# Optimization experiments

Hardware: AMD Instinct MI355X
Metric: run time of the kernel (lower is better)

Reference implementation:

```python
import jax, jax.numpy as jnp
import numpy as np

SINK = 4          # sink_size: tokens never evicted
MAX_CACHE = 8192  # sink_size + window_size
H = 32            # n_heads
HD = 128          # head_dim
D = H * HD        # d_model


def setup_inputs() -> dict:
    key = jax.random.key(0)
    ks = jax.random.split(key, 7)
    x = jax.random.normal(ks[0], (1, 1, D), dtype=jnp.float32)
    cached_k = jax.random.normal(ks[1], (1, H, MAX_CACHE, HD), dtype=jnp.float32)
    cached_v = jax.random.normal(ks[2], (1, H, MAX_CACHE, HD), dtype=jnp.float32)
    scale = 0.02
    Wq = jax.random.normal(ks[3], (D, D), dtype=jnp.float32) * scale
    Wk = jax.random.normal(ks[4], (D, D), dtype=jnp.float32) * scale
    Wv = jax.random.normal(ks[5], (D, D), dtype=jnp.float32) * scale
    Wo = jax.random.normal(ks[6], (D, D), dtype=jnp.float32) * scale
    return {"x": x, "cached_k": cached_k, "cached_v": cached_v,
            "Wq": Wq, "Wk": Wk, "Wv": Wv, "Wo": Wo}


def reference(x, cached_k, cached_v, Wq, Wk, Wv, Wo):
    """One StreamingLLM decode step with a full sink+window KV cache.

    x:        (1, 1, D)   single new token
    cached_k: (1, H, T, HD) with T == MAX_CACHE (cache at capacity)
    Returns (out, new_cached_k, new_cached_v) where out is (1, 1, D) and the
    new caches reflect sink-preserving eviction: [sink | recent[1:] | new].
    """
    B, S, _ = x.shape  # S == 1
    # projections for the new token -> (B, H, S, HD)
    q = (x @ Wq).reshape(B, S, H, HD).transpose(0, 2, 1, 3)
    k_new = (x @ Wk).reshape(B, S, H, HD).transpose(0, 2, 1, 3)
    v_new = (x @ Wv).reshape(B, S, H, HD).transpose(0, 2, 1, 3)

    # attend over past cache + new token (causal: single query sees everything)
    keys = jnp.concatenate([cached_k, k_new], axis=2)   # (B, H, T+1, HD)
    vals = jnp.concatenate([cached_v, v_new], axis=2)
    inv_sqrt_d = np.float32(1.0 / np.sqrt(HD))
    scores = jnp.einsum('bhqd,bhkd->bhqk', q, keys) * inv_sqrt_d
    attn = jax.nn.softmax(scores, axis=-1)
    ctx = jnp.einsum('bhqk,bhkd->bhqd', attn, vals)     # (B, H, 1, HD)
    out = ctx.transpose(0, 2, 1, 3).reshape(B, S, H * HD) @ Wo

    # KVCache.update full-cache branch: keep sink, drop oldest recent, append new
    new_cached_k = jnp.concatenate(
        [cached_k[:, :, :SINK], cached_k[:, :, SINK + 1:], k_new], axis=2)
    new_cached_v = jnp.concatenate(
        [cached_v[:, :, :SINK], cached_v[:, :, SINK + 1:], v_new], axis=2)
    return out, new_cached_k, new_cached_v
```

## Files before the change

kernel.cpp:

```cpp
#include <hip/hip_runtime.h>

#define D     4096
#define NH    32
#define HD    128
#define TT    8192
#define SINKN 4
#define NC    64
#define CS    (TT / NC)
#define ICH   32
#define ICHO  64

__global__ void qkv_partial(const float* __restrict__ x,
                            const float* __restrict__ Wq,
                            const float* __restrict__ Wk,
                            const float* __restrict__ Wv,
                            float* __restrict__ partA) {
    int bid = blockIdx.x;
    int mat = bid / 256;
    int rem = bid % 256;
    int jb  = rem >> 5;
    int ic  = rem & 31;
    const float* Wm = (mat == 0) ? Wq : (mat == 1) ? Wk : Wv;
    int tid = threadIdx.x;
    int j0  = jb * 512 + tid * 4;
    int i0  = ic * 128;
    __shared__ float xs[128];
    xs[tid] = x[i0 + tid];
    __syncthreads();
    float4 acc = {0.f, 0.f, 0.f, 0.f};
    const float* Wp = Wm + (size_t)i0 * D + j0;
    #pragma unroll 8
    for (int i = 0; i < 128; ++i) {
        float4 w = *(const float4*)Wp;
        float xv = xs[i];
        acc.x += xv * w.x; acc.y += xv * w.y;
        acc.z += xv * w.z; acc.w += xv * w.w;
        Wp += D;
    }
    *(float4*)(partA + (size_t)(mat * ICH + ic) * D + j0) = acc;
}

__global__ void attn_chunk(const float* __restrict__ partA,
                           const float* __restrict__ K,
                           const float* __restrict__ V,
                           float* __restrict__ newK,
                           float* __restrict__ newV,
                           float* __restrict__ partB) {
    int bid = blockIdx.x;
    int h = bid / NC;
    int c = bid % NC;
    int t0 = c * CS;
    int tid  = threadIdx.x;
    int wave = tid >> 6;
    int lane = tid & 63;
    int l31  = lane & 31;
    int half = lane >> 5;

    __shared__ float qs[HD];
    __shared__ float sc[CS];
    __shared__ float ml[2];
    __shared__ float ctx8[8][HD];

    {
        int d  = tid & 127;
        int hh = tid >> 7;
        const float* p = partA + (size_t)(hh * 16) * D + (size_t)h * HD + d;
        float s = 0.f;
        #pragma unroll
        for (int ic = 0; ic < 16; ++ic) s += p[(size_t)ic * D];
        ctx8[hh][d] = s;
    }
    __syncthreads();
    if (tid < HD) qs[tid] = ctx8[0][tid] + ctx8[1][tid];
    __syncthreads();

    float4 qv = *(const float4*)(qs + 4 * l31);
    const float scale = 0.08838834764831845f;

    const float* Kh = K    + (size_t)h * TT * HD;
    float*      nKh = newK + (size_t)h * TT * HD;
    for (int kk = 0; kk < 16; ++kk) {
        int r = t0 + kk * 8 + wave * 2 + half;
        float4 kv = *(const float4*)(Kh + (size_t)r * HD + 4 * l31);
        float p = qv.x * kv.x + qv.y * kv.y + qv.z * kv.z + qv.w * kv.w;
        p += __shfl_xor(p, 16, 64);
        p += __shfl_xor(p, 8, 64);
        p += __shfl_xor(p, 4, 64);
        p += __shfl_xor(p, 2, 64);
        p += __shfl_xor(p, 1, 64);
        if (l31 == 0) sc[r - t0] = p * scale;
        if (r != SINKN) {
            int dst = (r < SINKN) ? r : r - 1;
            *(float4*)(nKh + (size_t)dst * HD + 4 * l31) = kv;
        }
    }
    __syncthreads();
    if (wave == 0) {
        float s0 = sc[lane], s1 = sc[lane + 64];
        float m = fmaxf(s0, s1);
        #pragma unroll
        for (int off = 32; off; off >>= 1) m = fmaxf(m, __shfl_xor(m, off, 64));
        float w0 = __expf(s0 - m), w1 = __expf(s1 - m);
        sc[lane] = w0; sc[lane + 64] = w1;
        float l = w0 + w1;
        #pragma unroll
        for (int off = 32; off; off >>= 1) l += __shfl_xor(l, off, 64);
        if (lane == 0) { ml[0] = m; ml[1] = l; }
    }
    __syncthreads();
    const float* Vh = V    + (size_t)h * TT * HD;
    float*      nVh = newV + (size_t)h * TT * HD;
    float a0 = 0.f, a1 = 0.f, a2 = 0.f, a3 = 0.f;
    for (int kk = 0; kk < 16; ++kk) {
        int r = t0 + kk * 8 + wave * 2 + half;
        float4 vv = *(const float4*)(Vh + (size_t)r * HD + 4 * l31);
        float w = sc[r - t0];
        a0 += w * vv.x; a1 += w * vv.y; a2 += w * vv.z; a3 += w * vv.w;
        if (r != SINKN) {
            int dst = (r < SINKN) ? r : r - 1;
            *(float4*)(nVh + (size_t)dst * HD + 4 * l31) = vv;
        }
    }
    int g = wave * 2 + half;
    ctx8[g][4 * l31 + 0] = a0;
    ctx8[g][4 * l31 + 1] = a1;
    ctx8[g][4 * l31 + 2] = a2;
    ctx8[g][4 * l31 + 3] = a3;
    __syncthreads();
    float* pb = partB + ((size_t)h * NC + c) * (HD + 2);
    if (tid < HD) {
        float s = 0.f;
        #pragma unroll
        for (int gg = 0; gg < 8; ++gg) s += ctx8[gg][tid];
        pb[2 + tid] = s;
    }
    if (tid == 0) { pb[0] = ml[0]; pb[1] = ml[1]; }
}

__global__ void attn_combine(const float* __restrict__ partA,
                             const float* __restrict__ partB,
                             float* __restrict__ newK,
                             float* __restrict__ newV,
                             float* __restrict__ ctx) {
    int h = blockIdx.x;
    int tid = threadIdx.x;
    float qd = 0.f, kd = 0.f, vd = 0.f;
    const float* pq = partA + (size_t)h * HD + tid;
    #pragma unroll
    for (int ic = 0; ic < ICH; ++ic) {
        qd += pq[(size_t)ic * D];
        kd += pq[(size_t)(ICH + ic) * D];
        vd += pq[(size_t)(2 * ICH + ic) * D];
    }
    newK[((size_t)h * TT + (TT - 1)) * HD + tid] = kd;
    newV[((size_t)h * TT + (TT - 1)) * HD + tid] = vd;

    __shared__ float red[HD];
    __shared__ float marr[NC], larr[NC], earr[NC];
    red[tid] = qd * kd;
    __syncthreads();
    for (int s = 64; s > 0; s >>= 1) {
        if (tid < s) red[tid] += red[tid + s];
        __syncthreads();
    }
    float s_new = red[0] * 0.08838834764831845f;
    const float* pb = partB + (size_t)h * NC * (HD + 2);
    if (tid < NC) {
        marr[tid] = pb[(size_t)tid * (HD + 2)];
        larr[tid] = pb[(size_t)tid * (HD + 2) + 1];
    }
    __syncthreads();
    float M = s_new;
    for (int c = 0; c < NC; ++c) M = fmaxf(M, marr[c]);
    if (tid < NC) earr[tid] = __expf(marr[tid] - M);
    __syncthreads();
    float wn = __expf(s_new - M);
    float L = wn;
    for (int c = 0; c < NC; ++c) L += larr[c] * earr[c];
    float acc = wn * vd;
    for (int c = 0; c < NC; ++c)
        acc += earr[c] * pb[(size_t)c * (HD + 2) + 2 + tid];
    ctx[h * HD + tid] = acc / L;
}

__global__ void out_partial(const float* __restrict__ ctx,
                            const float* __restrict__ Wo,
                            float* __restrict__ partC) {
    int bid = blockIdx.x;
    int jb = bid >> 6;
    int ic = bid & 63;
    int tid = threadIdx.x;
    int j0 = jb * 512 + tid * 4;
    int i0 = ic * 64;
    __shared__ float xs[64];
    if (tid < 64) xs[tid] = ctx[i0 + tid];
    __syncthreads();
    float4 acc = {0.f, 0.f, 0.f, 0.f};
    const float* Wp = Wo + (size_t)i0 * D + j0;
    #pragma unroll 8
    for (int i = 0; i < 64; ++i) {
        float4 w = *(const float4*)Wp;
        float xv = xs[i];
        acc.x += xv * w.x; acc.y += xv * w.y;
        acc.z += xv * w.z; acc.w += xv * w.w;
        Wp += D;
    }
    *(float4*)(partC + (size_t)ic * D + j0) = acc;
}

__global__ void out_reduce(const float* __restrict__ partC,
                           float* __restrict__ out) {
    int j = blockIdx.x * 256 + threadIdx.x;
    float s = 0.f;
    #pragma unroll
    for (int ic = 0; ic < ICHO; ++ic) s += partC[(size_t)ic * D + j];
    out[j] = s;
}

extern "C" void kernel_launch(void* const* d_in, const int* in_sizes, int n_in,
                              void* d_out, int out_size, void* d_ws, size_t ws_size,
                              hipStream_t stream) {
    const float* x  = (const float*)d_in[0];
    const float* cK = (const float*)d_in[1];
    const float* cV = (const float*)d_in[2];
    const float* Wq = (const float*)d_in[3];
    const float* Wk = (const float*)d_in[4];
    const float* Wv = (const float*)d_in[5];
    const float* Wo = (const float*)d_in[6];

    float* out  = (float*)d_out;
    float* newK = out + D;
    float* newV = newK + (size_t)NH * TT * HD;

    float* ws    = (float*)d_ws;
    float* partA = ws;
    float* partB = partA + 3 * ICH * D;
    float* ctx   = partB + NH * NC * (HD + 2);

    qkv_partial <<<768,  128, 0, stream>>>(x, Wq, Wk, Wv, partA);
    attn_chunk  <<<NH * NC, 256, 0, stream>>>(partA, cK, cV, newK, newV, partB);
    attn_combine<<<NH,   HD,  0, stream>>>(partA, partB, newK, newV, ctx);
    out_partial <<<512,  128, 0, stream>>>(ctx, Wo, partA);
    out_reduce  <<<D / 256, 256, 0, stream>>>(partA, out);
}
```

Measured before the change: 189.9 us.

## Fuse attention combine and output reduction into fewer kernels using atomics

Reduces five launches to three. The new-token K/V write and its score now run in the c==0 block of attn_chunk and are stored as an extra partial. The combine step is folded into the output projection kernel, and the separate reduce kernel is replaced by atomicAdd into out, which qkv_partial zeroes first. The QKV split is also retiled to 64 input chunks with 256 threads per block. This removes launch overhead and intermediate round trips, at the cost of redundant softmax-combine work in every out_fused block and of atomic contention.

```diff
diff --git a/kernel.cpp b/kernel.cpp
--- a/kernel.cpp
+++ b/kernel.cpp
@@ -6,31 +6,34 @@
 #define TT    8192
 #define SINKN 4
 #define NC    64
-#define CS    (TT / NC)
-#define ICH   32
-#define ICHO  64
-
-__global__ void qkv_partial(const float* __restrict__ x,
-                            const float* __restrict__ Wq,
-                            const float* __restrict__ Wk,
-                            const float* __restrict__ Wv,
-                            float* __restrict__ partA) {
+#define CS    128
+#define ICH   64
+#define PBSTR (HD + 2)
+
+__global__ __launch_bounds__(256) void qkv_partial(
+        const float* __restrict__ x,
+        const float* __restrict__ Wq,
+        const float* __restrict__ Wk,
+        const float* __restrict__ Wv,
+        float* __restrict__ partA,
+        float* __restrict__ out) {
     int bid = blockIdx.x;
-    int mat = bid / 256;
-    int rem = bid % 256;
-    int jb  = rem >> 5;
-    int ic  = rem & 31;
+    int tid = threadIdx.x;
+    if (bid < 16) out[bid * 256 + tid] = 0.f;
+    int mat = bid >> 8;
+    int rem = bid & 255;
+    int jb  = rem >> 6;
+    int ic  = rem & 63;
     const float* Wm = (mat == 0) ? Wq : (mat == 1) ? Wk : Wv;
-    int tid = threadIdx.x;
-    int j0  = jb * 512 + tid * 4;
-    int i0  = ic * 128;
-    __shared__ float xs[128];
-    xs[tid] = x[i0 + tid];
+    int j0 = jb * 1024 + tid * 4;
+    int i0 = ic * 64;
+    __shared__ float xs[64];
+    if (tid < 64) xs[tid] = x[i0 + tid];
     __syncthreads();
     float4 acc = {0.f, 0.f, 0.f, 0.f};
     const float* Wp = Wm + (size_t)i0 * D + j0;
-    #pragma unroll 8
-    for (int i = 0; i < 128; ++i) {
+    #pragma unroll 16
+    for (int i = 0; i < 64; ++i) {
         float4 w = *(const float4*)Wp;
         float xv = xs[i];
         acc.x += xv * w.x; acc.y += xv * w.y;
@@ -40,15 +43,16 @@
     *(float4*)(partA + (size_t)(mat * ICH + ic) * D + j0) = acc;
 }
 
-__global__ void attn_chunk(const float* __restrict__ partA,
-                           const float* __restrict__ K,
-                           const float* __restrict__ V,
-                           float* __restrict__ newK,
-                           float* __restrict__ newV,
-                           float* __restrict__ partB) {
+__global__ __launch_bounds__(256) void attn_chunk(
+        const float* __restrict__ partA,
+        const float* __restrict__ K,
+        const float* __restrict__ V,
+        float* __restrict__ newK,
+        float* __restrict__ newV,
+        float* __restrict__ partB) {
     int bid = blockIdx.x;
-    int h = bid / NC;
-    int c = bid % NC;
+    int h = bid >> 6;
+    int c = bid & 63;
     int t0 = c * CS;
     int tid  = threadIdx.x;
     int wave = tid >> 6;
@@ -64,10 +68,10 @@
     {
         int d  = tid & 127;
         int hh = tid >> 7;
-        const float* p = partA + (size_t)(hh * 16) * D + (size_t)h * HD + d;
+        const float* p = partA + (size_t)(hh * 32) * D + (size_t)h * HD + d;
         float s = 0.f;
         #pragma unroll
-        for (int ic = 0; ic < 16; ++ic) s += p[(size_t)ic * D];
+        for (int i = 0; i < 32; ++i) s += p[(size_t)i * D];
         ctx8[hh][d] = s;
     }
     __syncthreads();
@@ -127,94 +131,99 @@
     ctx8[g][4 * l31 + 2] = a2;
     ctx8[g][4 * l31 + 3] = a3;
     __syncthreads();
-    float* pb = partB + ((size_t)h * NC + c) * (HD + 2);
+    float* pbE = partB + ((size_t)h * (NC + 1) + c) * PBSTR;
     if (tid < HD) {
         float s = 0.f;
         #pragma unroll
         for (int gg = 0; gg < 8; ++gg) s += ctx8[gg][tid];
-        pb[2 + tid] = s;
-    }
-    if (tid == 0) { pb[0] = ml[0]; pb[1] = ml[1]; }
-}
-
-__global__ void attn_combine(const float* __restrict__ partA,
-                             const float* __restrict__ partB,
-                             float* __restrict__ newK,
-                             float* __restrict__ newV,
-                             float* __restrict__ ctx) {
-    int h = blockIdx.x;
-    int tid = threadIdx.x;
-    float qd = 0.f, kd = 0.f, vd = 0.f;
-    const float* pq = partA + (size_t)h * HD + tid;
-    #pragma unroll
-    for (int ic = 0; ic < ICH; ++ic) {
-        qd += pq[(size_t)ic * D];
-        kd += pq[(size_t)(ICH + ic) * D];
-        vd += pq[(size_t)(2 * ICH + ic) * D];
-    }
-    newK[((size_t)h * TT + (TT - 1)) * HD + tid] = kd;
-    newV[((size_t)h * TT + (TT - 1)) * HD + tid] = vd;
-
-    __shared__ float red[HD];
-    __shared__ float marr[NC], larr[NC], earr[NC];
-    red[tid] = qd * kd;
-    __syncthreads();
-    for (int s = 64; s > 0; s >>= 1) {
-        if (tid < s) red[tid] += red[tid + s];
+        pbE[2 + tid] = s;
+    }
+    if (tid == 0) { pbE[0] = ml[0]; pbE[1] = ml[1]; }
+
+    if (c == 0) {
+        float kd = 0.f, vd = 0.f;
+        if (tid < HD) {
+            const float* pk = partA + (size_t)(ICH) * D + (size_t)h * HD + tid;
+            const float* pv = partA + (size_t)(2 * ICH) * D + (size_t)h * HD + tid;
+            #pragma unroll
+            for (int i = 0; i < ICH; ++i) {
+                kd += pk[(size_t)i * D];
+                vd += pv[(size_t)i * D];
+            }
+            newK[((size_t)h * TT + (TT - 1)) * HD + tid] = kd;
+            newV[((size_t)h * TT + (TT - 1)) * HD + tid] = vd;
+        }
         __syncthreads();
-    }
-    float s_new = red[0] * 0.08838834764831845f;
-    const float* pb = partB + (size_t)h * NC * (HD + 2);
-    if (tid < NC) {
-        marr[tid] = pb[(size_t)tid * (HD + 2)];
-        larr[tid] = pb[(size_t)tid * (HD + 2) + 1];
-    }
-    __syncthreads();
-    float M = s_new;
-    for (int c = 0; c < NC; ++c) M = fmaxf(M, marr[c]);
-    if (tid < NC) earr[tid] = __expf(marr[tid] - M);
-    __syncthreads();
-    float wn = __expf(s_new - M);
-    float L = wn;
-    for (int c = 0; c < NC; ++c) L += larr[c] * earr[c];
-    float acc = wn * vd;
-    for (int c = 0; c < NC; ++c)
-        acc += earr[c] * pb[(size_t)c * (HD + 2) + 2 + tid];
-    ctx[h * HD + tid] = acc / L;
-}
-
-__global__ void out_partial(const float* __restrict__ ctx,
-                            const float* __restrict__ Wo,
-                            float* __restrict__ partC) {
+        if (tid < HD) ctx8[0][tid] = qs[tid] * kd;
+        __syncthreads();
+        float* pbN = partB + ((size_t)h * (NC + 1) + NC) * PBSTR;
+        if (tid < 64) {
+            float s = ctx8[0][tid] + ctx8[0][tid + 64];
+            #pragma unroll
+            for (int off = 32; off; off >>= 1) s += __shfl_xor(s, off, 64);
+            if (tid == 0) { pbN[0] = s * scale; pbN[1] = 1.0f; }
+        }
+        if (tid < HD) pbN[2 + tid] = vd;
+    }
+}
+
+__global__ __launch_bounds__(128) void out_fused(
+        const float* __restrict__ partB,
+        const float* __restrict__ Wo,
+        float* __restrict__ out) {
     int bid = blockIdx.x;
     int jb = bid >> 6;
     int ic = bid & 63;
     int tid = threadIdx.x;
+    int h  = ic >> 1;
+    int d0 = (ic & 1) * 64;
+
+    __shared__ float marr[NC + 1], larr[NC + 1], wgt[NC + 1];
+    __shared__ float ctx[64];
+    __shared__ float Ls;
+
+    const float* pb = partB + (size_t)h * (NC + 1) * PBSTR;
+    if (tid <= NC) {
+        marr[tid] = pb[tid * PBSTR];
+        larr[tid] = pb[tid * PBSTR + 1];
+    }
+    __syncthreads();
+    float M = marr[0];
+    #pragma unroll
+    for (int cc = 1; cc <= NC; ++cc) M = fmaxf(M, marr[cc]);
+    if (tid <= NC) wgt[tid] = __expf(marr[tid] - M);
+    __syncthreads();
+    if (tid < 64) {
+        float s = wgt[tid] * larr[tid] + ((tid == 0) ? wgt[NC] * larr[NC] : 0.f);
+        #pragma unroll
+        for (int off = 32; off; off >>= 1) s += __shfl_xor(s, off, 64);
+        if (tid == 0) Ls = s;
+    }
+    __syncthreads();
+    if (tid < 64) {
+        const float* pc = pb + 2 + d0 + tid;
+        float acc = 0.f;
+        #pragma unroll
+        for (int cc = 0; cc <= NC; ++cc) acc += wgt[cc] * pc[cc * PBSTR];
+        ctx[tid] = acc / Ls;
+    }
+    __syncthreads();
+
     int j0 = jb * 512 + tid * 4;
-    int i0 = ic * 64;
-    __shared__ float xs[64];
-    if (tid < 64) xs[tid] = ctx[i0 + tid];
-    __syncthreads();
     float4 acc = {0.f, 0.f, 0.f, 0.f};
-    const float* Wp = Wo + (size_t)i0 * D + j0;
-    #pragma unroll 8
+    const float* Wp = Wo + (size_t)(ic * 64) * D + j0;
+    #pragma unroll 16
     for (int i = 0; i < 64; ++i) {
         float4 w = *(const float4*)Wp;
-        float xv = xs[i];
+        float xv = ctx[i];
         acc.x += xv * w.x; acc.y += xv * w.y;
         acc.z += xv * w.z; acc.w += xv * w.w;
         Wp += D;
     }
-    *(float4*)(partC + (size_t)ic * D + j0) = acc;
-}
-
-__global__ void out_reduce(const float* __restrict__ partC,
-                           float* __restrict__ out) {
-    int j = blockIdx.x * 256 + threadIdx.x;
-    float s = 0.f;
-    #pragma unroll
-    for (int ic = 0; ic < ICHO; ++ic) s += partC[(size_t)ic * D + j];
-    out[j] = s;
+    atomicAdd(&out[j0 + 0], acc.x);
+    atomicAdd(&out[j0 + 1], acc.y);
+    atomicAdd(&out[j0 + 2], acc.z);
+    atomicAdd(&out[j0 + 3], acc.w);
 }
 
 extern "C" void kernel_launch(void* const* d_in, const int* in_sizes, int n_in,
@@ -235,11 +244,8 @@
     float* ws    = (float*)d_ws;
     float* partA = ws;
     float* partB = partA + 3 * ICH * D;
-    float* ctx   = partB + NH * NC * (HD + 2);
-
-    qkv_partial <<<768,  128, 0, stream>>>(x, Wq, Wk, Wv, partA);
-    attn_chunk  <<<NH * NC, 256, 0, stream>>>(partA, cK, cV, newK, newV, partB);
-    attn_combine<<<NH,   HD,  0, stream>>>(partA, partB, newK, newV, ctx);
-    out_partial <<<512,  128, 0, stream>>>(ctx, Wo, partA);
-    out_reduce  <<<D / 256, 256, 0, stream>>>(partA, out);
-}
+
+    qkv_partial<<<768,     256, 0, stream>>>(x, Wq, Wk, Wv, partA, out);
+    attn_chunk <<<NH * NC, 256, 0, stream>>>(partA, cK, cV, newK, newV, partB);
+    out_fused  <<<512,     128, 0, stream>>>(partB, Wo, out);
+}
```

New measurement: 182.4 us. 4.0% less time.
